# Optimization experiments

Measured on AMD Instinct MI355X. Metric: run time of the kernel, lower is better.

Reference implementation:

```python
import jax, jax.numpy as jnp
import numpy as np

B, C, N, D, K, M, E, G = 2, 64, 16384, 3, 128, 1, 262144, 3


def setup_inputs() -> dict:
    key = jax.random.key(0)
    ks = jax.random.split(key, 15)
    scale = 1.0 / (C * C)
    return {
        "x": jax.random.normal(ks[0], (B, C, N), jnp.float32),
        "nodes": jax.random.uniform(ks[1], (B, N, D), jnp.float32),
        "node_weights": jax.random.uniform(ks[2], (B, N, M), jnp.float32),
        "geo": jax.random.normal(ks[3], (B, G, N), jnp.float32),
        "directed_edges": jax.random.randint(ks[4], (B, E, 2), 0, N, jnp.int32),
        "edge_gradient_weights": 0.1 * jax.random.normal(ks[5], (B, E, D), jnp.float32),
        "modes": jax.random.normal(ks[6], (K, D, M), jnp.float32),
        "weights_c": scale * jax.random.uniform(ks[7], (C, C, K, M), jnp.float32),
        "weights_s": scale * jax.random.uniform(ks[8], (C, C, K, M), jnp.float32),
        "weights_0": scale * jax.random.uniform(ks[9], (C, C, 1, M), jnp.float32),
        "W": jax.random.normal(ks[10], (C, C), jnp.float32) / np.sqrt(C),
        "gw": jax.random.normal(ks[11], (C, C * D), jnp.float32) / np.sqrt(C * D),
        "geo_wx": jax.random.normal(ks[12], (C, G), jnp.float32) / np.sqrt(G),
        "wx": jax.random.normal(ks[13], (C, C), jnp.float32) / np.sqrt(C),
        "w2": jax.random.normal(ks[14], (C, C), jnp.float32) / np.sqrt(C),
    }


def reference(x, nodes, node_weights, geo, directed_edges, edge_gradient_weights,
              modes, weights_c, weights_s, weights_0, W, gw, geo_wx, wx, w2):
    # ---- Fourier bases: cos(kx), sin(kx), 1 -------------------------------
    temp = jnp.einsum('bxd,kdw->bxkw', nodes, modes)          # [B,N,K,M]
    bases_c, bases_s = jnp.cos(temp), jnp.sin(temp)
    b, n = temp.shape[0], temp.shape[1]
    bases_0 = jnp.ones((b, n, 1, temp.shape[3]), temp.dtype)
    nw = node_weights[:, :, None, :]                          # quadrature weights
    wb_c, wb_s, wb_0 = bases_c * nw, bases_s * nw, bases_0 * nw

    # ---- Spectral convolution (non-uniform Fourier neural layer) ----------
    x_c = jnp.einsum('bix,bxkw->bikw', x, wb_c)
    x_s = -jnp.einsum('bix,bxkw->bikw', x, wb_s)
    x_0 = jnp.einsum('bix,bxkw->bikw', x, wb_0)
    f_c = jnp.einsum('bikw,iokw->bokw', x_c, weights_c) - jnp.einsum('bikw,iokw->bokw', x_s, weights_s)
    f_s = jnp.einsum('bikw,iokw->bokw', x_s, weights_c) + jnp.einsum('bikw,iokw->bokw', x_c, weights_s)
    f_0 = jnp.einsum('bikw,iokw->bokw', x_0, weights_0)
    x1 = (jnp.einsum('bokw,bxkw->box', f_0, bases_0)
          + 2.0 * jnp.einsum('bokw,bxkw->box', f_c, bases_c)
          - 2.0 * jnp.einsum('bokw,bxkw->box', f_s, bases_s))

    # ---- Pointwise linear W ----------------------------------------------
    x2 = jnp.einsum('oi,bix->box', W, x)

    # ---- Least-squares gradient via edge gather + scatter-add -------------
    fT = jnp.transpose(x, (0, 2, 1))                          # [B,N,C]
    tgt, src = directed_edges[..., 0], directed_edges[..., 1]  # [B,E]
    f_src = jnp.take_along_axis(fT, src[:, :, None], axis=1)   # [B,E,C]
    f_tgt = jnp.take_along_axis(fT, tgt[:, :, None], axis=1)
    df = f_src - f_tgt
    # message[b,e,c,d] = w[b,e,d] * df[b,e,c], flattened c-major -> [B,E,C*D]
    msg = (df[..., :, None] * edge_gradient_weights[..., None, :]).reshape(b, tgt.shape[1], -1)
    gradf = jnp.zeros((b, n, msg.shape[-1]), msg.dtype).at[jnp.arange(b)[:, None], tgt].add(msg)
    x3 = jnp.einsum('og,bng->bon', gw, gradf)                  # [B,C,N]

    # ---- Geo embedding: w2 @ (softsign(geo_wx@geo) * (wx@x)) --------------
    h = jax.nn.soft_sign(jnp.einsum('og,bgx->box', geo_wx, geo)) * jnp.einsum('oi,bix->box', wx, x)
    x4 = jnp.einsum('oi,bix->box', w2, h)

    return jax.nn.gelu(x1 + x2 + x3 + x4, approximate=False)
```

## Files before the change

kernel.cpp:

```cpp
#include <hip/hip_runtime.h>
#include <hip/hip_fp16.h>
#include <math.h>

#define BB 2
#define CC 64
#define NN 16384
#define DD 3
#define KK 128
#define EE 262144
#define GG 3
#define PP 128
#define PP2 64
#define LL (NN/PP)
#define KTOT 576

typedef short bf16x8 __attribute__((ext_vector_type(8)));
typedef float f32x4  __attribute__((ext_vector_type(4)));

__device__ __forceinline__ short f2bf(float f) {
    unsigned u = __float_as_uint(f);
    u += 0x7FFF + ((u >> 16) & 1);
    return (short)(u >> 16);
}
__device__ __forceinline__ float bf2f(unsigned short u) {
    return __uint_as_float(((unsigned)u) << 16);
}

constexpr size_t OFF_XB   = 0;
constexpr size_t OFF_PC   = OFF_XB   + (size_t)BB*NN*32;
constexpr size_t OFF_PS   = OFF_PC   + (size_t)BB*PP*CC*KK;
constexpr size_t OFF_BIN4 = OFF_PC;
constexpr size_t OFF_AC   = OFF_PS   + (size_t)BB*PP*CC*KK;
constexpr size_t OFF_AS   = OFF_AC   + (size_t)BB*CC*KK;
constexpr size_t OFF_F0   = OFF_AS   + (size_t)BB*CC*KK;
constexpr size_t OFF_X0   = OFF_F0   + (size_t)BB*CC;
constexpr size_t OFF_CNT  = OFF_X0   + (size_t)BB*CC;
constexpr size_t OFF_OFFS = OFF_CNT  + (size_t)BB*NN;
constexpr size_t OFF_RANK = OFF_OFFS + (size_t)BB*NN;
constexpr size_t OFF_GRB  = OFF_RANK + (size_t)BB*EE;
constexpr size_t OFF_APAN = OFF_GRB  + (size_t)BB*NN*96;
constexpr size_t OFF_GWXT = OFF_APAN + (size_t)BB*KTOT*CC/2;

#define S_A0 (BB*(NN/64))
#define S_A1 (S_A0 + BB*CC)
#define S_A2 (S_A1 + (BB*EE)/256)
#define S_A3 (S_A2 + 48)
#define S_A4 (S_A3 + BB*PP2*4)
__global__ void __launch_bounds__(256) k1(const float* __restrict__ x,
                                          const float* __restrict__ nwt,
                                          const int* __restrict__ edges,
                                          const float* __restrict__ W,
                                          const float* __restrict__ gw,
                                          const float* __restrict__ geo_wx,
                                          const float* __restrict__ w2,
                                          const float* __restrict__ nodes,
                                          const float* __restrict__ modes,
                                          unsigned short* __restrict__ xB,
                                          float* __restrict__ x0,
                                          int* __restrict__ counts,
                                          int* __restrict__ rank,
                                          float* __restrict__ gwxT,
                                          short* __restrict__ ApanB,
                                          float* __restrict__ pc,
                                          float* __restrict__ ps) {
    int blk = blockIdx.x;
    int tid = threadIdx.x;
    __shared__ __align__(16) char smem[36864];
    if (blk < S_A0) {
        float (*tile)[65] = (float (*)[65])smem;
        int b = blk / (NN/64);
        int n0 = (blk % (NN/64)) * 64;
        int c = tid & 63, r4 = tid >> 6;
        for (int rr = 0; rr < 16; rr++) {
            int i = r4*16 + rr;
            tile[i][c] = x[((size_t)b*CC + i)*NN + n0 + c];
        }
        __syncthreads();
        for (int rr = 0; rr < 16; rr++) {
            int nn = r4*16 + rr;
            xB[((size_t)b*NN + n0 + nn)*64 + c] = (unsigned short)f2bf(tile[c][nn]);
        }
    } else if (blk < S_A1) {
        float* red = (float*)smem;
        int bi = blk - S_A0;
        int b = bi >> 6, i = bi & 63;
        const float4* __restrict__ xr = (const float4*)&x[((size_t)b*CC + i)*NN];
        const float4* __restrict__ wr = (const float4*)&nwt[(size_t)b*NN];
        float s = 0.f;
        for (int t = tid; t < NN/4; t += 256) {
            float4 xv = xr[t];
            float4 wv = wr[t];
            s += xv.x*wv.x + xv.y*wv.y + xv.z*wv.z + xv.w*wv.w;
        }
        red[tid] = s;
        __syncthreads();
        for (int off = 128; off > 0; off >>= 1) {
            if (tid < off) red[tid] += red[tid+off];
            __syncthreads();
        }
        if (tid == 0) x0[b*CC + i] = red[0];
    } else if (blk < S_A2) {
        int idx = (blk - S_A1)*256 + tid;
        int tgt = edges[(size_t)idx*2 + 0];
        int b = idx / EE;
        rank[idx] = atomicAdd(&counts[b*NN + tgt], 1);
    } else if (blk < S_A3) {
        int idx = (blk - S_A2)*256 + tid;
        if (idx < CC*CC) {
            int j = idx>>6, o = idx&63;
            short wv  = f2bf(W[o*CC+j]);
            short w2v = f2bf(w2[o*CC+j]);
            ApanB[((size_t)(0*CC+o))*KTOT + 256 + j] = wv;
            ApanB[((size_t)(1*CC+o))*KTOT + 256 + j] = wv;
            ApanB[((size_t)(0*CC+o))*KTOT + 320 + j] = w2v;
            ApanB[((size_t)(1*CC+o))*KTOT + 320 + j] = w2v;
        }
        if (idx < CC*CC*DD) {
            int g = idx>>6, o = idx&63;
            short gv = f2bf(gw[o*(CC*DD)+g]);
            ApanB[((size_t)(0*CC+o))*KTOT + 384 + g] = gv;
            ApanB[((size_t)(1*CC+o))*KTOT + 384 + g] = gv;
        }
        if (idx < GG*CC) { int g = idx>>6, i = idx&63; gwxT[idx] = geo_wx[i*GG+g]; }
    } else {
        short* Axw = (short*)smem;
        short* Bc  = (short*)(smem + 17408);
        short* Bsn = (short*)(smem + 17408 + 8704);
        float* ndl = (float*)(smem + 17408 + 8704 + 8704);
        int bc = blk - S_A3;
        int b = bc >> 8;
        int rem = bc & 255;
        int chunk2 = rem >> 2;
        int kt = rem & 3;
        int k0 = kt * 32;
        int lane = tid & 63;
        int w = tid >> 6;
        int col = lane & 15;
        int quad = lane >> 4;
        int wk = w & 1;
        int wi = w >> 1;

        f32x4 ac[2], as4[2];
#pragma unroll
        for (int it = 0; it < 2; it++)
#pragma unroll
            for (int r = 0; r < 4; r++) { ac[it][r] = 0.f; as4[it][r] = 0.f; }

        for (int h = 0; h < 2; h++) {
            int nbase = chunk2*256 + h*128;
            if (h) __syncthreads();
            for (int e = tid; e < 128*3; e += 256) ndl[e] = nodes[((size_t)b*NN + nbase)*3 + e];
#pragma unroll
            for (int s = 0; s < 8; s++) {
                int e = tid + s*256;
                int i = e >> 5, seg = e & 31;
                float4 xv = *(const float4*)&x[((size_t)b*CC + i)*NN + nbase + seg*4];
                float4 wv = *(const float4*)&nwt[(size_t)b*NN + nbase + seg*4];
                unsigned lo = (unsigned)(unsigned short)f2bf(xv.x*wv.x)
                            | ((unsigned)(unsigned short)f2bf(xv.y*wv.y) << 16);
                unsigned hi = (unsigned)(unsigned short)f2bf(xv.z*wv.z)
                            | ((unsigned)(unsigned short)f2bf(xv.w*wv.w) << 16);
                *(uint2*)&Axw[i*136 + seg*4] = make_uint2(lo, hi);
            }
            __syncthreads();
#pragma unroll
            for (int s = 0; s < 16; s++) {
                int e = tid + s*256;
                int n = e & 127, kl = e >> 7;
                int k = k0 + kl;
                float t = ndl[n*3+0]*modes[k*3+0] + ndl[n*3+1]*modes[k*3+1]
                        + ndl[n*3+2]*modes[k*3+2];
                Bc [kl*136 + n] = f2bf(__cosf(t));
                Bsn[kl*136 + n] = f2bf(__sinf(t));
            }
            __syncthreads();

            int rowB = (wk*16 + col)*136;
#pragma unroll
            for (int ns = 0; ns < 4; ns++) {
                int koff = ns*32 + quad*8;
                bf16x8 bcf = *(bf16x8*)&Bc [rowB + koff];
                bf16x8 bsf = *(bf16x8*)&Bsn[rowB + koff];
#pragma unroll
                for (int it = 0; it < 2; it++) {
                    int itile = wi*2 + it;
                    bf16x8 af = *(bf16x8*)&Axw[(itile*16 + col)*136 + koff];
                    ac[it]  = __builtin_amdgcn_mfma_f32_16x16x32_bf16(af, bcf, ac[it], 0, 0, 0);
                    as4[it] = __builtin_amdgcn_mfma_f32_16x16x32_bf16(af, bsf, as4[it], 0, 0, 0);
                }
            }
        }
        int base = (b*PP2 + chunk2)*CC;
        int kw = k0 + wk*16 + col;
#pragma unroll
        for (int it = 0; it < 2; it++) {
#pragma unroll
            for (int r = 0; r < 4; r++) {
                int i = (wi*2 + it)*16 + quad*4 + r;
                pc[(size_t)(base + i)*KK + kw] = ac[it][r];
                ps[(size_t)(base + i)*KK + kw] = as4[it][r];
            }
        }
    }
}

__global__ void __launch_bounds__(256) k2(const float* __restrict__ pc, const float* __restrict__ ps,
                                          float* __restrict__ Ac, float* __restrict__ As,
                                          const int* __restrict__ counts,
                                          int* __restrict__ offsets) {
    int blk = blockIdx.x;
    int tid = threadIdx.x;
    if (blk < 256) {
        int idx = blk*64 + (tid >> 2);
        int sub = tid & 3;
        if (idx >= BB*CC*KK) return;
        int b = idx / (CC*KK);
        int r = idx % (CC*KK);
        float sc = 0.f, ss = 0.f;
        for (int ch = sub; ch < PP2; ch += 4) {
            size_t o = ((size_t)(b*PP2 + ch)*CC)*KK + r;
            sc += pc[o]; ss += ps[o];
        }
        sc += __shfl_xor(sc, 1); sc += __shfl_xor(sc, 2);
        ss += __shfl_xor(ss, 1); ss += __shfl_xor(ss, 2);
        if (sub == 0) { Ac[idx] = sc; As[idx] = ss; }
    } else {
        int b = blk - 256;
        __shared__ int part[256];
        int base = b*NN + tid*64;
        int s = 0;
        for (int j = 0; j < 64; j++) s += counts[base + j];
        part[tid] = s;
        __syncthreads();
        for (int off = 1; off < 256; off <<= 1) {
            int v = (tid >= off) ? part[tid - off] : 0;
            __syncthreads();
            part[tid] += v;
            __syncthreads();
        }
        int excl = part[tid] - s;
        for (int j = 0; j < 64; j++) {
            int c = counts[base + j];
            offsets[base + j] = excl;
            excl += c;
        }
    }
}

__global__ void __launch_bounds__(256) k3(const float* __restrict__ Ac, const float* __restrict__ As_,
                                          const float* __restrict__ wc, const float* __restrict__ wsw,
                                          const float* __restrict__ w0, const float* __restrict__ x0,
                                          const int* __restrict__ edges, const float* __restrict__ egw,
                                          const int* __restrict__ offs, const int* __restrict__ rank,
                                          float4* __restrict__ bin4,
                                          short* __restrict__ ApanB, float* __restrict__ f0) {
    int idx = blockIdx.x;
    int tid = threadIdx.x;
    if (idx >= BB*CC*2) {
        int e = (idx - BB*CC*2)*256 + tid;
        int b = e / EE;
        int tgt = edges[(size_t)e*2+0];
        int src = edges[(size_t)e*2+1];
        const float* __restrict__ ew = &egw[(size_t)e*3];
        float e0 = ew[0], e1 = ew[1], e2 = ew[2];
        int pos = offs[b*NN+tgt] + rank[e];
        bin4[(size_t)b*EE + pos] = make_float4(__int_as_float(src), e0, e1, e2);
        return;
    }
    int b = idx / (CC*2);
    int rem = idx % (CC*2);
    int o = rem >> 1, khalf = rem & 1;
    int kl = tid & 63, ig = tid >> 6;
    int k = khalf*64 + kl;
    float fc = 0.f, fs = 0.f;
    for (int ii = 0; ii < 16; ii++) {
        int i = ig*16 + ii;
        float a_c = Ac[(b*CC+i)*KK + k];
        float a_s = As_[(b*CC+i)*KK + k];
        float wcc = wc[((size_t)(i*CC+o))*KK + k];
        float wss = wsw[((size_t)(i*CC+o))*KK + k];
        fc += a_c*wcc + a_s*wss;
        fs += a_c*wss - a_s*wcc;
    }
    __shared__ float rc[256], rs[256];
    __shared__ float f0s[64];
    rc[tid] = fc; rs[tid] = fs;
    if (khalf == 0 && tid < 64) f0s[tid] = x0[b*CC + tid] * w0[tid*CC + o];
    __syncthreads();
    if (ig == 0) {
        fc = rc[kl] + rc[64+kl] + rc[128+kl] + rc[192+kl];
        fs = rs[kl] + rs[64+kl] + rs[128+kl] + rs[192+kl];
        unsigned pk = (unsigned)(unsigned short)f2bf(2.f*fc)
                    | ((unsigned)(unsigned short)f2bf(-2.f*fs) << 16);
        ((unsigned*)ApanB)[((size_t)(b*CC + o))*(KTOT/2) + k] = pk;
    }
    if (khalf == 0 && tid == 0) {
        float acc = 0.f;
        for (int i = 0; i < 64; i++) acc += f0s[i];
        f0[b*CC+o] = acc;
    }
}

__global__ void __launch_bounds__(256) k_eg(const unsigned short* __restrict__ xB,
                                            const int* __restrict__ offsets,
                                            const float4* __restrict__ bin4,
                                            const float* __restrict__ nodes,
                                            const float* __restrict__ modes,
                                            const float* __restrict__ geo,
                                            const short* __restrict__ ApanB,
                                            const float* __restrict__ f0,
                                            const float* __restrict__ wx,
                                            const float* __restrict__ gwxT,
                                            float* __restrict__ out) {
    int blk = blockIdx.x;
    int b  = blk >> 9;
    int n0 = (blk & 511) * 32;
    int tid = threadIdx.x;
    int lane = tid & 63;
    int w = tid >> 6;
    int w16 = w * 16;
    int col  = lane & 15;
    int quad = lane >> 4;
    int quad8 = quad * 8;
    int quad4 = quad * 4;

    __shared__ __align__(16) char smem[37776];
    short* As = (short*)smem;
    short* Bs = (short*)(smem + 9216);
    short* Ws = (short*)(smem + 13824);
    unsigned short* gradfL = (unsigned short*)(smem + 23040);
    float* ndl  = (float*)(smem + 36864);
    float* geo3 = (float*)(smem + 37248);
    int* soff   = (int*)(smem + 37632);

    if (tid < 96) ndl[tid]  = nodes[((size_t)b*NN + n0)*3 + tid];
    if (tid < 96) geo3[tid] = geo[((size_t)b*GG + (tid >> 5))*NN + n0 + (tid & 31)];
    if (tid < 33) {
        int idx = n0 + tid;
        soff[tid] = (idx < NN) ? offsets[b*NN + idx] : EE;
    }
    for (int e = tid; e < 4096; e += 256) {
        int i = e >> 6, j = e & 63;
        Ws[i*72 + j] = f2bf(wx[i*64 + j]);
    }
    f32x4 acc[2], xwa[2];
    float f0v[4];
#pragma unroll
    for (int r = 0; r < 4; r++) f0v[r] = f0[b*CC + w16 + quad4 + r];
#pragma unroll
    for (int nt = 0; nt < 2; nt++) {
#pragma unroll
        for (int r = 0; r < 4; r++) { acc[nt][r] = f0v[r]; xwa[nt][r] = 0.f; }
    }
    __syncthreads();

    const unsigned short* __restrict__ xBb = xB + (size_t)b*NN*64 + lane;
    const float4* __restrict__ binb = bin4 + (size_t)b*EE;
    for (int q = 0; q < 8; q++) {
        int nl = w*8 + q;
        int js = soff[nl], je = soff[nl+1];
        float a0 = 0.f, a1 = 0.f, a2 = 0.f, s0 = 0.f, s1 = 0.f, s2 = 0.f;
#pragma unroll 8
        for (int j = js; j < je; j++) {
            float4 e = binb[j];
            int src = __float_as_int(e.x);
            float xs = bf2f(xBb[(size_t)src*64]);
            a0 = fmaf(xs, e.y, a0);
            a1 = fmaf(xs, e.z, a1);
            a2 = fmaf(xs, e.w, a2);
            s0 += e.y; s1 += e.z; s2 += e.w;
        }
        float xtgt = bf2f(xBb[(size_t)(n0 + nl)*64]);
        float fv0 = a0 - xtgt*s0;
        float fv1 = a1 - xtgt*s1;
        float fv2 = a2 - xtgt*s2;
        int g0 = lane*3;
        gradfL[(g0>>6)*2304 + nl*72 + (g0&63)] = (unsigned short)f2bf(fv0);
        int g1 = g0 + 1;
        gradfL[(g1>>6)*2304 + nl*72 + (g1&63)] = (unsigned short)f2bf(fv1);
        int g2 = g0 + 2;
        gradfL[(g2>>6)*2304 + nl*72 + (g2&63)] = (unsigned short)f2bf(fv2);
    }

    const short* __restrict__ Ab = ApanB + ((size_t)b*CC)*KTOT;

    for (int c = 0; c < 9; c++) {
        __syncthreads();
        for (int e = tid; e < 512; e += 256) {
            int o = e >> 3, seg = e & 7;
            *(uint4*)&As[o*72 + seg*8] =
                *(const uint4*)&Ab[(size_t)o*KTOT + c*64 + seg*8];
        }
        if (c < 4) {
#pragma unroll
            for (int s = 0; s < 4; s++) {
                int e = tid + s*256;
                int n = e >> 5, kpl = e & 31;
                int kp = c*32 + kpl;
                float t = ndl[n*3+0]*modes[kp*3+0] + ndl[n*3+1]*modes[kp*3+1]
                        + ndl[n*3+2]*modes[kp*3+2];
                unsigned pk = (unsigned)(unsigned short)f2bf(__cosf(t))
                            | ((unsigned)(unsigned short)f2bf(__sinf(t)) << 16);
                ((unsigned*)Bs)[n*36 + kpl] = pk;
            }
        } else if (c == 4) {
            {
                int e = tid;
                int n = e >> 3, seg = e & 7;
                *(uint4*)&Bs[n*72 + seg*8] =
                    *(const uint4*)&xB[((size_t)(b*NN + n0 + n))*64 + seg*8];
            }
        } else if (c == 5) {
#pragma unroll
            for (int r = 0; r < 4; r++) {
                int i = w16 + quad4 + r;
                float g0 = gwxT[i], g1 = gwxT[64+i], g2 = gwxT[128+i];
#pragma unroll
                for (int nt = 0; nt < 2; nt++) {
                    int n = nt*16 + col;
                    float t = g0*geo3[n] + g1*geo3[32+n] + g2*geo3[64+n];
                    float ssv = t / (1.f + fabsf(t));
                    Bs[n*72 + i] = f2bf(ssv * xwa[nt][r]);
                }
            }
        }
        __syncthreads();
        const short* Bbase = (c >= 6) ? (const short*)&gradfL[(size_t)(c-6)*2304] : Bs;
        int rowA = (w16 + col) * 72;
#pragma unroll
        for (int ko = 0; ko < 2; ko++) {
            int koff = ko*32 + quad8;
            bf16x8 af = *(bf16x8*)&As[rowA + koff];
            if (c == 4) {
                bf16x8 wf = *(bf16x8*)&Ws[rowA + koff];
#pragma unroll
                for (int nt = 0; nt < 2; nt++) {
                    bf16x8 bfv = *(bf16x8*)&Bbase[(nt*16 + col)*72 + koff];
                    acc[nt] = __builtin_amdgcn_mfma_f32_16x16x32_bf16(af, bfv, acc[nt], 0, 0, 0);
                    xwa[nt] = __builtin_amdgcn_mfma_f32_16x16x32_bf16(wf, bfv, xwa[nt], 0, 0, 0);
                }
            } else {
#pragma unroll
                for (int nt = 0; nt < 2; nt++) {
                    bf16x8 bfv = *(bf16x8*)&Bbase[(nt*16 + col)*72 + koff];
                    acc[nt] = __builtin_amdgcn_mfma_f32_16x16x32_bf16(af, bfv, acc[nt], 0, 0, 0);
                }
            }
        }
    }
#pragma unroll
    for (int nt = 0; nt < 2; nt++) {
#pragma unroll
        for (int r = 0; r < 4; r++) {
            int o = w16 + quad4 + r;
            float v = acc[nt][r];
            float g = 0.5f * v * (1.f + erff(v * 0.70710678118654752f));
            out[((size_t)b*CC + o)*NN + n0 + nt*16 + col] = g;
        }
    }
}

extern "C" void kernel_launch(void* const* d_in, const int* in_sizes, int n_in,
                              void* d_out, int out_size, void* d_ws, size_t ws_size,
                              hipStream_t stream) {
    const float* x      = (const float*)d_in[0];
    const float* nodes  = (const float*)d_in[1];
    const float* nwt    = (const float*)d_in[2];
    const float* geo    = (const float*)d_in[3];
    const int*   edges  = (const int*)d_in[4];
    const float* egw    = (const float*)d_in[5];
    const float* modes  = (const float*)d_in[6];
    const float* wc     = (const float*)d_in[7];
    const float* wsw    = (const float*)d_in[8];
    const float* w0     = (const float*)d_in[9];
    const float* W      = (const float*)d_in[10];
    const float* gw     = (const float*)d_in[11];
    const float* geo_wx = (const float*)d_in[12];
    const float* wx     = (const float*)d_in[13];
    const float* w2     = (const float*)d_in[14];

    float* ws   = (float*)d_ws;
    unsigned short* xB  = (unsigned short*)(ws + OFF_XB);
    float* pc   = ws + OFF_PC;
    float* ps   = ws + OFF_PS;
    float* Ac   = ws + OFF_AC;
    float* As_  = ws + OFF_AS;
    float* f0   = ws + OFF_F0;
    float* x0   = ws + OFF_X0;
    int*  counts = (int*)(ws + OFF_CNT);
    int*  offs   = (int*)(ws + OFF_OFFS);
    int*  rank   = (int*)(ws + OFF_RANK);
    float4* bin4 = (float4*)(ws + OFF_BIN4);
    short* ApanB  = (short*)(ws + OFF_APAN);
    float* gwxT   = ws + OFF_GWXT;
    float* out  = (float*)d_out;

    hipMemsetAsync(counts, 0, (size_t)(BB*NN)*sizeof(int), stream);

    k1 <<<S_A4, 256, 0, stream>>>(x, nwt, edges, W, gw, geo_wx, w2, nodes, modes,
                                  xB, x0, counts, rank, gwxT, ApanB, pc, ps);
    k2 <<<256 + BB, 256, 0, stream>>>(pc, ps, Ac, As_, counts, offs);
    k3 <<<BB*CC*2 + (BB*EE)/256, 256, 0, stream>>>(Ac, As_, wc, wsw, w0, x0,
                                                   edges, egw, offs, rank, bin4, ApanB, f0);
    k_eg <<<BB*(NN/32), 256, 0, stream>>>(xB, offs, bin4, nodes, modes, geo,
                                          ApanB, f0, wx, gwxT, out);
}
```

Measured before the change: 198.6 us.

## Double k_eg block to 512 threads with 2x4 wave tiling of output

The final fused kernel now runs 8 waves per block instead of 4. Waves are arranged as 4 row groups by 2 column groups, so each wave computes one 16x16 MFMA tile instead of two. Each wave also handles 4 gather nodes instead of 8. The aim is more latency hiding for the irregular edge gather and less serial work per wave. The cost is more waves competing for the same LDS and barriers, plus a tighter register budget from launch_bounds(512,8).

```diff
diff --git a/kernel.cpp b/kernel.cpp
--- a/kernel.cpp
+++ b/kernel.cpp
@@ -301,24 +301,25 @@
     }
 }
 
-__global__ void __launch_bounds__(256) k_eg(const unsigned short* __restrict__ xB,
-                                            const int* __restrict__ offsets,
-                                            const float4* __restrict__ bin4,
-                                            const float* __restrict__ nodes,
-                                            const float* __restrict__ modes,
-                                            const float* __restrict__ geo,
-                                            const short* __restrict__ ApanB,
-                                            const float* __restrict__ f0,
-                                            const float* __restrict__ wx,
-                                            const float* __restrict__ gwxT,
-                                            float* __restrict__ out) {
+__global__ void __launch_bounds__(512, 8) k_eg(const unsigned short* __restrict__ xB,
+                                               const int* __restrict__ offsets,
+                                               const float4* __restrict__ bin4,
+                                               const float* __restrict__ nodes,
+                                               const float* __restrict__ modes,
+                                               const float* __restrict__ geo,
+                                               const short* __restrict__ ApanB,
+                                               const float* __restrict__ f0,
+                                               const float* __restrict__ wx,
+                                               const float* __restrict__ gwxT,
+                                               float* __restrict__ out) {
     int blk = blockIdx.x;
     int b  = blk >> 9;
     int n0 = (blk & 511) * 32;
     int tid = threadIdx.x;
     int lane = tid & 63;
     int w = tid >> 6;
-    int w16 = w * 16;
+    int wr = w >> 1;
+    int wc = w & 1;
     int col  = lane & 15;
     int quad = lane >> 4;
     int quad8 = quad * 8;
@@ -335,32 +336,26 @@
 
     if (tid < 96) ndl[tid]  = nodes[((size_t)b*NN + n0)*3 + tid];
     if (tid < 96) geo3[tid] = geo[((size_t)b*GG + (tid >> 5))*NN + n0 + (tid & 31)];
-    if (tid < 33) {
-        int idx = n0 + tid;
-        soff[tid] = (idx < NN) ? offsets[b*NN + idx] : EE;
-    }
-    for (int e = tid; e < 4096; e += 256) {
+    if (tid >= 128 && tid < 161) {
+        int idx = n0 + tid - 128;
+        soff[tid - 128] = (idx < NN) ? offsets[b*NN + idx] : EE;
+    }
+    for (int e = tid; e < 4096; e += 512) {
         int i = e >> 6, j = e & 63;
         Ws[i*72 + j] = f2bf(wx[i*64 + j]);
     }
-    f32x4 acc[2], xwa[2];
-    float f0v[4];
-#pragma unroll
-    for (int r = 0; r < 4; r++) f0v[r] = f0[b*CC + w16 + quad4 + r];
-#pragma unroll
-    for (int nt = 0; nt < 2; nt++) {
-#pragma unroll
-        for (int r = 0; r < 4; r++) { acc[nt][r] = f0v[r]; xwa[nt][r] = 0.f; }
-    }
+    f32x4 acc, xwa;
+#pragma unroll
+    for (int r = 0; r < 4; r++) { acc[r] = f0[b*CC + wr*16 + quad4 + r]; xwa[r] = 0.f; }
     __syncthreads();
 
     const unsigned short* __restrict__ xBb = xB + (size_t)b*NN*64 + lane;
     const float4* __restrict__ binb = bin4 + (size_t)b*EE;
-    for (int q = 0; q < 8; q++) {
-        int nl = w*8 + q;
+    for (int q = 0; q < 4; q++) {
+        int nl = w*4 + q;
         int js = soff[nl], je = soff[nl+1];
         float a0 = 0.f, a1 = 0.f, a2 = 0.f, s0 = 0.f, s1 = 0.f, s2 = 0.f;
-#pragma unroll 8
+#pragma unroll 4
         for (int j = js; j < je; j++) {
             float4 e = binb[j];
             int src = __float_as_int(e.x);
@@ -386,15 +381,15 @@
 
     for (int c = 0; c < 9; c++) {
         __syncthreads();
-        for (int e = tid; e < 512; e += 256) {
-            int o = e >> 3, seg = e & 7;
+        {
+            int o = tid >> 3, seg = tid & 7;
             *(uint4*)&As[o*72 + seg*8] =
                 *(const uint4*)&Ab[(size_t)o*KTOT + c*64 + seg*8];
         }
         if (c < 4) {
 #pragma unroll
-            for (int s = 0; s < 4; s++) {
-                int e = tid + s*256;
+            for (int s = 0; s < 2; s++) {
+                int e = tid + s*512;
                 int n = e >> 5, kpl = e & 31;
                 int kp = c*32 + kpl;
                 float t = ndl[n*3+0]*modes[kp*3+0] + ndl[n*3+1]*modes[kp*3+1]
@@ -404,59 +399,44 @@
                 ((unsigned*)Bs)[n*36 + kpl] = pk;
             }
         } else if (c == 4) {
-            {
-                int e = tid;
-                int n = e >> 3, seg = e & 7;
+            if (tid < 256) {
+                int n = tid >> 3, seg = tid & 7;
                 *(uint4*)&Bs[n*72 + seg*8] =
                     *(const uint4*)&xB[((size_t)(b*NN + n0 + n))*64 + seg*8];
             }
         } else if (c == 5) {
+            int n = wc*16 + col;
+            float gv0 = geo3[n], gv1 = geo3[32+n], gv2 = geo3[64+n];
 #pragma unroll
             for (int r = 0; r < 4; r++) {
-                int i = w16 + quad4 + r;
-                float g0 = gwxT[i], g1 = gwxT[64+i], g2 = gwxT[128+i];
-#pragma unroll
-                for (int nt = 0; nt < 2; nt++) {
-                    int n = nt*16 + col;
-                    float t = g0*geo3[n] + g1*geo3[32+n] + g2*geo3[64+n];
-                    float ssv = t / (1.f + fabsf(t));
-                    Bs[n*72 + i] = f2bf(ssv * xwa[nt][r]);
-                }
+                int i = wr*16 + quad4 + r;
+                float t = gwxT[i]*gv0 + gwxT[64+i]*gv1 + gwxT[128+i]*gv2;
+                float ssv = t / (1.f + fabsf(t));
+                Bs[n*72 + i] = f2bf(ssv * xwa[r]);
             }
         }
         __syncthreads();
         const short* Bbase = (c >= 6) ? (const short*)&gradfL[(size_t)(c-6)*2304] : Bs;
-        int rowA = (w16 + col) * 72;
+        int rowA = (wr*16 + col) * 72;
+        int rowB = (wc*16 + col) * 72;
 #pragma unroll
         for (int ko = 0; ko < 2; ko++) {
             int koff = ko*32 + quad8;
             bf16x8 af = *(bf16x8*)&As[rowA + koff];
+            bf16x8 bfv = *(bf16x8*)&Bbase[rowB + koff];
+            acc = __builtin_amdgcn_mfma_f32_16x16x32_bf16(af, bfv, acc, 0, 0, 0);
             if (c == 4) {
                 bf16x8 wf = *(bf16x8*)&Ws[rowA + koff];
-#pragma unroll
-                for (int nt = 0; nt < 2; nt++) {
-                    bf16x8 bfv = *(bf16x8*)&Bbase[(nt*16 + col)*72 + koff];
-                    acc[nt] = __builtin_amdgcn_mfma_f32_16x16x32_bf16(af, bfv, acc[nt], 0, 0, 0);
-                    xwa[nt] = __builtin_amdgcn_mfma_f32_16x16x32_bf16(wf, bfv, xwa[nt], 0, 0, 0);
-                }
-            } else {
-#pragma unroll
-                for (int nt = 0; nt < 2; nt++) {
-                    bf16x8 bfv = *(bf16x8*)&Bbase[(nt*16 + col)*72 + koff];
-                    acc[nt] = __builtin_amdgcn_mfma_f32_16x16x32_bf16(af, bfv, acc[nt], 0, 0, 0);
-                }
-            }
-        }
-    }
-#pragma unroll
-    for (int nt = 0; nt < 2; nt++) {
-#pragma unroll
-        for (int r = 0; r < 4; r++) {
-            int o = w16 + quad4 + r;
-            float v = acc[nt][r];
-            float g = 0.5f * v * (1.f + erff(v * 0.70710678118654752f));
-            out[((size_t)b*CC + o)*NN + n0 + nt*16 + col] = g;
-        }
+                xwa = __builtin_amdgcn_mfma_f32_16x16x32_bf16(wf, bfv, xwa, 0, 0, 0);
+            }
+        }
+    }
+#pragma unroll
+    for (int r = 0; r < 4; r++) {
+        int o = wr*16 + quad4 + r;
+        float v = acc[r];
+        float g = 0.5f * v * (1.f + erff(v * 0.70710678118654752f));
+        out[((size_t)b*CC + o)*NN + n0 + wc*16 + col] = g;
     }
 }
 
@@ -502,6 +482,6 @@
     k2 <<<256 + BB, 256, 0, stream>>>(pc, ps, Ac, As_, counts, offs);
     k3 <<<BB*CC*2 + (BB*EE)/256, 256, 0, stream>>>(Ac, As_, wc, wsw, w0, x0,
                                                    edges, egw, offs, rank, bin4, ApanB, f0);
-    k_eg <<<BB*(NN/32), 256, 0, stream>>>(xB, offs, bin4, nodes, modes, geo,
+    k_eg <<<BB*(NN/32), 512, 0, stream>>>(xB, offs, bin4, nodes, modes, geo,
                                           ApanB, f0, wx, gwxT, out);
 }
```

Measured after the change: 184.7 us, median of 2. 1.08x faster.
